# Performance work log

Measured on AMD Instinct MI355X. Metric: run time of the kernel, lower is better.

Reference implementation:

```python
import jax, jax.numpy as jnp
import numpy as np

N_NODES = 50000
N_EDGES = 800000
NFEAT = 128
NHID = 64
NLAYER = 3
BN_EPS = 1e-5


def _bn(h, gamma, beta):
    # BatchNorm1d, training-mode batch statistics (biased variance)
    mu = jnp.mean(h, axis=0)
    var = jnp.mean((h - mu) ** 2, axis=0)
    return gamma * (h - mu) * jax.lax.rsqrt(var + BN_EPS) + beta


def setup_inputs() -> dict:
    key = jax.random.key(0)
    ks = jax.random.split(key, 8)
    x = jax.random.normal(ks[0], (N_NODES, NFEAT), dtype=jnp.float32)
    edge_index = jax.random.randint(ks[1], (2, N_EDGES), 0, N_NODES, dtype=jnp.int64)
    # transform: Linear(nfeat, nhid) with bias, then BN
    W_t = jax.random.normal(ks[2], (NFEAT, NHID), dtype=jnp.float32) / np.sqrt(NFEAT)
    b_t = jnp.zeros((NHID,), dtype=jnp.float32)
    g_t = jnp.ones((NHID,), dtype=jnp.float32)
    bb_t = jnp.zeros((NHID,), dtype=jnp.float32)
    # per-layer GIN MLPs (bias=False) and BN affine params, stacked over layers
    W1 = jax.random.normal(ks[3], (NLAYER, NHID, NHID), dtype=jnp.float32) / np.sqrt(NHID)
    W2 = jax.random.normal(ks[4], (NLAYER, NHID, NHID), dtype=jnp.float32) / np.sqrt(NHID)
    gamma = jnp.ones((NLAYER, NHID), dtype=jnp.float32)
    beta = jnp.zeros((NLAYER, NHID), dtype=jnp.float32)
    return {"x": x, "edge_index": edge_index, "W_t": W_t, "b_t": b_t,
            "g_t": g_t, "bb_t": bb_t, "W1": W1, "W2": W2,
            "gamma": gamma, "beta": beta}


def reference(x, edge_index, W_t, b_t, g_t, bb_t, W1, W2, gamma, beta):
    src, dst = edge_index[0], edge_index[1]
    # input transform: Linear + BN
    h = _bn(x @ W_t + b_t, g_t, bb_t)
    for i in range(NLAYER):
        # dropout p=0 -> identity
        # GINConv (eps=0): (1+eps)*h + sum_{j->i} h_j, then 2-layer MLP
        agg = h + jax.ops.segment_sum(h[src], dst, num_segments=N_NODES)
        h = jax.nn.relu(agg @ W1[i]) @ W2[i]
        h = jax.nn.relu(h)
        h = _bn(h, gamma[i], beta[i])
    # per-graph boolean-mask split is a pure partition of rows; return full matrix
    return h
```

## Files before the change

### kernel.cpp

```cpp
#include <hip/hip_runtime.h>

#define NND 50000
#define NED 800000
#define NF  128
#define NH  64
#define BN_EPS 1e-5
#define NCOPY 64
#define SCB  256
#define NSB  ((NND + SCB - 1) / SCB)

#define WS_HA     0
#define WS_STATS  12800000
#define WS_SSF    (WS_STATS + NCOPY*128*8)
#define WS_DEG    (WS_SSF + 512)
#define WS_OFFS   (WS_DEG + NND*4)
#define WS_CUR    (WS_OFFS + (NND+4)*4)
#define WS_PARTS  (WS_CUR + NND*4)
#define WS_ESRC   (WS_PARTS + 256*4)

__global__ void k_deg(const int* __restrict__ dst, int* __restrict__ deg) {
    int e4 = blockIdx.x * 256 + threadIdx.x;
    if (e4 * 4 < NED) {
        int4 d = ((const int4*)dst)[e4];
        atomicAdd(&deg[d.x], 1);
        atomicAdd(&deg[d.y], 1);
        atomicAdd(&deg[d.z], 1);
        atomicAdd(&deg[d.w], 1);
    }
}

__global__ __launch_bounds__(SCB) void k_part(const int* __restrict__ deg,
                                              int* __restrict__ offs,
                                              int* __restrict__ parts) {
    __shared__ int sd[SCB];
    int t = threadIdx.x;
    int i = blockIdx.x * SCB + t;
    int v = (i < NND) ? deg[i] : 0;
    sd[t] = v;
    __syncthreads();
#pragma unroll
    for (int off = 1; off < SCB; off <<= 1) {
        int u = (t >= off) ? sd[t - off] : 0;
        __syncthreads();
        sd[t] += u;
        __syncthreads();
    }
    if (i < NND) offs[i] = sd[t] - v;
    if (t == SCB - 1) parts[blockIdx.x] = sd[t];
}

__global__ __launch_bounds__(256) void k_scan2(int* __restrict__ parts) {
    __shared__ int sd[256];
    int t = threadIdx.x;
    int v = (t < NSB) ? parts[t] : 0;
    sd[t] = v;
    __syncthreads();
#pragma unroll
    for (int off = 1; off < 256; off <<= 1) {
        int u = (t >= off) ? sd[t - off] : 0;
        __syncthreads();
        sd[t] += u;
        __syncthreads();
    }
    if (t < NSB) parts[t] = sd[t] - v;
}

__global__ __launch_bounds__(256) void k_apply(int* __restrict__ offs,
                                               const int* __restrict__ parts,
                                               int* __restrict__ cur) {
    int i = blockIdx.x * 256 + threadIdx.x;
    if (i < NND) {
        int o = offs[i] + parts[i >> 8];
        offs[i] = o;
        cur[i] = o;
    }
    if (i == NND) offs[NND] = NED;
}

__global__ void k_fill(const int* __restrict__ src, const int* __restrict__ dst,
                       int* __restrict__ cur, int* __restrict__ esrc) {
    int e4 = blockIdx.x * 256 + threadIdx.x;
    if (e4 * 4 < NED) {
        int4 d = ((const int4*)dst)[e4];
        int4 s = ((const int4*)src)[e4];
        esrc[atomicAdd(&cur[d.x], 1)] = s.x;
        esrc[atomicAdd(&cur[d.y], 1)] = s.y;
        esrc[atomicAdd(&cur[d.z], 1)] = s.z;
        esrc[atomicAdd(&cur[d.w], 1)] = s.w;
    }
}

__global__ void k_fin(double* __restrict__ st,
                      const float* __restrict__ g, const float* __restrict__ b,
                      float* __restrict__ ssout) {
    int c = threadIdx.x;
    double sum = 0.0, ssq = 0.0;
    for (int cp = 0; cp < NCOPY; ++cp) {
        sum += st[cp * 128 + c];
        ssq += st[cp * 128 + 64 + c];
    }
    for (int cp = 0; cp < NCOPY; ++cp) {
        st[cp * 128 + c] = 0.0;
        st[cp * 128 + 64 + c] = 0.0;
    }
    double mu  = sum / (double)NND;
    double var = ssq / (double)NND - mu * mu;
    if (var < 0.0) var = 0.0;
    double rs = 1.0 / sqrt(var + BN_EPS);
    double sc = (double)g[c] * rs;
    ssout[c]      = (float)sc;
    ssout[64 + c] = (float)((double)b[c] - mu * sc);
}

__global__ __launch_bounds__(128) void k_transform(const float* __restrict__ x,
                                                   const float* __restrict__ Wt,
                                                   const float* __restrict__ bt,
                                                   float* __restrict__ outraw,
                                                   double* __restrict__ stats) {
    __shared__ __align__(16) float Wl[NF * NH];
    __shared__ __align__(16) float sTbuf[2 * 64 * 68];
    int tid  = threadIdx.x;
    int wave = tid >> 6, lane = tid & 63;
    int ti = lane & 7, tj = lane >> 3;
    int tile = blockIdx.x * 2 + wave;
    int base = tile * 64;
    float* sTw = &sTbuf[wave * 64 * 68];
    const float4* x4 = (const float4*)x;

#pragma unroll
    for (int r = 0; r < 16; ++r) {
        int i4 = r * 128 + tid;
        ((float4*)Wl)[i4] = ((const float4*)Wt)[i4];
    }

    float acc[8][8];
#pragma unroll
    for (int i = 0; i < 8; ++i)
#pragma unroll
        for (int j = 0; j < 8; ++j) acc[i][j] = 0.f;

    for (int ch = 0; ch < 2; ++ch) {
        __syncthreads();
#pragma unroll
        for (int s = 0; s < 16; ++s) {
            int flat = s * 64 + lane;
            int nl = flat >> 4, q = flat & 15;
            float4 v = {0.f, 0.f, 0.f, 0.f};
            if (base + nl < NND) v = x4[(size_t)(base + nl) * 32 + ch * 16 + q];
            sTw[(q * 4 + 0) * 68 + nl] = v.x;
            sTw[(q * 4 + 1) * 68 + nl] = v.y;
            sTw[(q * 4 + 2) * 68 + nl] = v.z;
            sTw[(q * 4 + 3) * 68 + nl] = v.w;
        }
        __syncthreads();
#pragma unroll 2
        for (int k = 0; k < 64; ++k) {
            const float* ap = &sTw[k * 68 + ti * 8];
            float4 alo = *(const float4*)ap;
            float4 ahi = *(const float4*)(ap + 4);
            const float* wp = &Wl[(ch * 64 + k) * NH + tj * 8];
            float4 wlo = *(const float4*)wp;
            float4 whi = *(const float4*)(wp + 4);
            float a8[8] = {alo.x, alo.y, alo.z, alo.w, ahi.x, ahi.y, ahi.z, ahi.w};
            float w8[8] = {wlo.x, wlo.y, wlo.z, wlo.w, whi.x, whi.y, whi.z, whi.w};
#pragma unroll
            for (int i = 0; i < 8; ++i)
#pragma unroll
                for (int j = 0; j < 8; ++j) acc[i][j] += a8[i] * w8[j];
        }
    }

    float b8[8];
    *(float4*)&b8[0] = ((const float4*)bt)[tj * 2];
    *(float4*)&b8[4] = ((const float4*)bt)[tj * 2 + 1];

    float s8[8], q8[8];
#pragma unroll
    for (int j = 0; j < 8; ++j) { s8[j] = 0.f; q8[j] = 0.f; }
#pragma unroll
    for (int i = 0; i < 8; ++i) {
        int n = base + ti * 8 + i;
        if (n < NND) {
            float o[8];
#pragma unroll
            for (int j = 0; j < 8; ++j) {
                o[j] = acc[i][j] + b8[j];
                s8[j] += o[j];
                q8[j] += o[j] * o[j];
            }
            *(float4*)&outraw[(size_t)n * NH + tj * 8]     = *(float4*)&o[0];
            *(float4*)&outraw[(size_t)n * NH + tj * 8 + 4] = *(float4*)&o[4];
        }
    }
#pragma unroll
    for (int m = 1; m < 8; m <<= 1) {
#pragma unroll
        for (int j = 0; j < 8; ++j) {
            s8[j] += __shfl_xor(s8[j], m);
            q8[j] += __shfl_xor(q8[j], m);
        }
    }
    if (ti == 0) {
        int slot = (tile & (NCOPY - 1)) * 128 + tj * 8;
#pragma unroll
        for (int j = 0; j < 8; ++j) {
            atomicAdd(&stats[slot + j], (double)s8[j]);
            atomicAdd(&stats[slot + 64 + j], (double)q8[j]);
        }
    }
}

__global__ __launch_bounds__(256) void k_agg(const float* __restrict__ inraw,
                                             float* __restrict__ aggout,
                                             const float* __restrict__ ss,
                                             const int* __restrict__ offs,
                                             const int* __restrict__ esrc) {
    int tid  = threadIdx.x;
    int lane = tid & 63;
    int wv   = tid >> 6;
    int n = blockIdx.x * 4 + wv;
    int q = lane & 15;
    int r = lane >> 4;
    const float4* in4 = (const float4*)inraw;

    int e0 = offs[n], e1 = offs[n + 1];
    int deg = e1 - e0;

    float4 self = make_float4(0.f, 0.f, 0.f, 0.f);
    if (r == 0) self = in4[(size_t)n * 16 + q];

    float ax = 0.f, ay = 0.f, az = 0.f, aw = 0.f;
    for (int bb = e0; bb < e1; bb += 64) {
        int m = e1 - bb; if (m > 64) m = 64;
        int idx = (lane < m) ? esrc[bb + lane] : 0;
        int t = 0;
        for (; t + 16 <= m; t += 16) {
            int j0 = __shfl(idx, t + r);
            int j1 = __shfl(idx, t + 4 + r);
            int j2 = __shfl(idx, t + 8 + r);
            int j3 = __shfl(idx, t + 12 + r);
            float4 v0 = in4[(size_t)j0 * 16 + q];
            float4 v1 = in4[(size_t)j1 * 16 + q];
            float4 v2 = in4[(size_t)j2 * 16 + q];
            float4 v3 = in4[(size_t)j3 * 16 + q];
            ax += (v0.x + v1.x) + (v2.x + v3.x);
            ay += (v0.y + v1.y) + (v2.y + v3.y);
            az += (v0.z + v1.z) + (v2.z + v3.z);
            aw += (v0.w + v1.w) + (v2.w + v3.w);
        }
        for (; t < m; t += 4) {
            int e = t + r;
            int j = __shfl(idx, e & 63);
            if (e < m) {
                float4 v = in4[(size_t)j * 16 + q];
                ax += v.x; ay += v.y; az += v.z; aw += v.w;
            }
        }
    }

    ax += __shfl_xor(ax, 16); ay += __shfl_xor(ay, 16);
    az += __shfl_xor(az, 16); aw += __shfl_xor(aw, 16);
    ax += __shfl_xor(ax, 32); ay += __shfl_xor(ay, 32);
    az += __shfl_xor(az, 32); aw += __shfl_xor(aw, 32);

    if (r == 0) {
        float4 sc4 = ((const float4*)ss)[q];
        float4 sh4 = ((const float4*)(ss + 64))[q];
        float dn = (float)(deg + 1);
        float4 res;
        res.x = sc4.x * (ax + self.x) + dn * sh4.x;
        res.y = sc4.y * (ay + self.y) + dn * sh4.y;
        res.z = sc4.z * (az + self.z) + dn * sh4.z;
        res.w = sc4.w * (aw + self.w) + dn * sh4.w;
        ((float4*)aggout)[(size_t)n * 16 + q] = res;
    }
}

__global__ __launch_bounds__(128) void k_mlp(float* __restrict__ h,
                                             double* __restrict__ statsout,
                                             const float* __restrict__ W1,
                                             const float* __restrict__ W2) {
    __shared__ __align__(16) float W1l[NH * NH];
    __shared__ __align__(16) float W2l[NH * NH];
    __shared__ __align__(16) float sTbuf[2 * 64 * 68];
    int tid  = threadIdx.x;
    int wave = tid >> 6, lane = tid & 63;
    int ti = lane & 7, tj = lane >> 3;
    int tile = blockIdx.x * 2 + wave;
    int base = tile * 64;
    float* sTw = &sTbuf[wave * 64 * 68];
    const float4* h4 = (const float4*)h;

#pragma unroll
    for (int r = 0; r < 8; ++r) {
        int i4 = r * 128 + tid;
        ((float4*)W1l)[i4] = ((const float4*)W1)[i4];
        ((float4*)W2l)[i4] = ((const float4*)W2)[i4];
    }
#pragma unroll
    for (int s = 0; s < 16; ++s) {
        int flat = s * 64 + lane;
        int nl = flat >> 4, q = flat & 15;
        float4 v = {0.f, 0.f, 0.f, 0.f};
        if (base + nl < NND) v = h4[(size_t)(base + nl) * 16 + q];
        sTw[(q * 4 + 0) * 68 + nl] = v.x;
        sTw[(q * 4 + 1) * 68 + nl] = v.y;
        sTw[(q * 4 + 2) * 68 + nl] = v.z;
        sTw[(q * 4 + 3) * 68 + nl] = v.w;
    }
    __syncthreads();

    float acc[8][8];
#pragma unroll
    for (int i = 0; i < 8; ++i)
#pragma unroll
        for (int j = 0; j < 8; ++j) acc[i][j] = 0.f;
#pragma unroll 2
    for (int k = 0; k < 64; ++k) {
        const float* ap = &sTw[k * 68 + ti * 8];
        float4 alo = *(const float4*)ap;
        float4 ahi = *(const float4*)(ap + 4);
        const float* wp = &W1l[k * NH + tj * 8];
        float4 wlo = *(const float4*)wp;
        float4 whi = *(const float4*)(wp + 4);
        float a8[8] = {alo.x, alo.y, alo.z, alo.w, ahi.x, ahi.y, ahi.z, ahi.w};
        float w8[8] = {wlo.x, wlo.y, wlo.z, wlo.w, whi.x, whi.y, whi.z, whi.w};
#pragma unroll
        for (int i = 0; i < 8; ++i)
#pragma unroll
            for (int j = 0; j < 8; ++j) acc[i][j] += a8[i] * w8[j];
    }
#pragma unroll
    for (int i = 0; i < 8; ++i)
#pragma unroll
        for (int j = 0; j < 8; ++j) acc[i][j] = fmaxf(acc[i][j], 0.f);

    __syncthreads();
#pragma unroll
    for (int j = 0; j < 8; ++j) {
        float* p = &sTw[(tj * 8 + j) * 68 + ti * 8];
        float4 lo = {acc[0][j], acc[1][j], acc[2][j], acc[3][j]};
        float4 hi = {acc[4][j], acc[5][j], acc[6][j], acc[7][j]};
        *(float4*)p = lo;
        *(float4*)(p + 4) = hi;
    }
    __syncthreads();

    float a2[8][8];
#pragma unroll
    for (int i = 0; i < 8; ++i)
#pragma unroll
        for (int j = 0; j < 8; ++j) a2[i][j] = 0.f;
#pragma unroll 2
    for (int k = 0; k < 64; ++k) {
        const float* ap = &sTw[k * 68 + ti * 8];
        float4 alo = *(const float4*)ap;
        float4 ahi = *(const float4*)(ap + 4);
        const float* wp = &W2l[k * NH + tj * 8];
        float4 wlo = *(const float4*)wp;
        float4 whi = *(const float4*)(wp + 4);
        float a8[8] = {alo.x, alo.y, alo.z, alo.w, ahi.x, ahi.y, ahi.z, ahi.w};
        float w8[8] = {wlo.x, wlo.y, wlo.z, wlo.w, whi.x, whi.y, whi.z, whi.w};
#pragma unroll
        for (int i = 0; i < 8; ++i)
#pragma unroll
            for (int j = 0; j < 8; ++j) a2[i][j] += a8[i] * w8[j];
    }

    float s8[8], q8[8];
#pragma unroll
    for (int j = 0; j < 8; ++j) { s8[j] = 0.f; q8[j] = 0.f; }
#pragma unroll
    for (int i = 0; i < 8; ++i) {
        int n = base + ti * 8 + i;
        if (n < NND) {
            float o[8];
#pragma unroll
            for (int j = 0; j < 8; ++j) {
                o[j] = fmaxf(a2[i][j], 0.f);
                s8[j] += o[j];
                q8[j] += o[j] * o[j];
            }
            *(float4*)&h[(size_t)n * NH + tj * 8]     = *(float4*)&o[0];
            *(float4*)&h[(size_t)n * NH + tj * 8 + 4] = *(float4*)&o[4];
        }
    }
#pragma unroll
    for (int m = 1; m < 8; m <<= 1) {
#pragma unroll
        for (int j = 0; j < 8; ++j) {
            s8[j] += __shfl_xor(s8[j], m);
            q8[j] += __shfl_xor(q8[j], m);
        }
    }
    if (ti == 0) {
        int slot = (tile & (NCOPY - 1)) * 128 + tj * 8;
#pragma unroll
        for (int j = 0; j < 8; ++j) {
            atomicAdd(&statsout[slot + j], (double)s8[j]);
            atomicAdd(&statsout[slot + 64 + j], (double)q8[j]);
        }
    }
}

__global__ void k_bnout(float* __restrict__ h, const float* __restrict__ ss) {
    int i4 = blockIdx.x * 256 + threadIdx.x;
    if (i4 < NND * NH / 4) {
        int cg = i4 & 15;
        float4 v   = ((float4*)h)[i4];
        float4 scv = ((const float4*)ss)[cg];
        float4 shv = ((const float4*)(ss + 64))[cg];
        v.x = v.x * scv.x + shv.x;
        v.y = v.y * scv.y + shv.y;
        v.z = v.z * scv.z + shv.z;
        v.w = v.w * scv.w + shv.w;
        ((float4*)h)[i4] = v;
    }
}

extern "C" void kernel_launch(void* const* d_in, const int* in_sizes, int n_in,
                              void* d_out, int out_size, void* d_ws, size_t ws_size,
                              hipStream_t stream) {
    const float* x     = (const float*)d_in[0];
    const int*   ei    = (const int*)d_in[1];
    const float* Wt    = (const float*)d_in[2];
    const float* bt    = (const float*)d_in[3];
    const float* gt    = (const float*)d_in[4];
    const float* bbt   = (const float*)d_in[5];
    const float* W1    = (const float*)d_in[6];
    const float* W2    = (const float*)d_in[7];
    const float* gamma = (const float*)d_in[8];
    const float* beta  = (const float*)d_in[9];
    float* out = (float*)d_out;

    char* ws = (char*)d_ws;
    float*  hA    = (float*)(ws + WS_HA);
    double* stats = (double*)(ws + WS_STATS);
    float*  ssf   = (float*)(ws + WS_SSF);
    int*    deg   = (int*)(ws + WS_DEG);
    int*    offs  = (int*)(ws + WS_OFFS);
    int*    cur   = (int*)(ws + WS_CUR);
    int*    parts = (int*)(ws + WS_PARTS);
    int*    esrc  = (int*)(ws + WS_ESRC);

    const int* srcv = ei;
    const int* dstv = ei + NED;

    hipMemsetAsync(stats, 0, NCOPY * 128 * 8 + 512 + NND * 4, stream);

    const int EB4 = (NED / 4 + 255) / 256;
    k_deg<<<EB4, 256, 0, stream>>>(dstv, deg);
    k_part<<<NSB, SCB, 0, stream>>>(deg, offs, parts);
    k_scan2<<<1, 256, 0, stream>>>(parts);
    k_apply<<<NSB, 256, 0, stream>>>(offs, parts, cur);
    k_fill<<<EB4, 256, 0, stream>>>(srcv, dstv, cur, esrc);

    const int NT2 = 391;
    const int NB  = NND / 4;

    k_transform<<<NT2, 128, 0, stream>>>(x, Wt, bt, hA, stats);
    k_fin<<<1, 64, 0, stream>>>(stats, gt, bbt, ssf);

    k_agg<<<NB, 256, 0, stream>>>(hA, out, ssf, offs, esrc);
    k_mlp<<<NT2, 128, 0, stream>>>(out, stats, W1, W2);
    k_fin<<<1, 64, 0, stream>>>(stats, gamma, beta, ssf);

    k_agg<<<NB, 256, 0, stream>>>(out, hA, ssf, offs, esrc);
    k_mlp<<<NT2, 128, 0, stream>>>(hA, stats, W1 + 4096, W2 + 4096);
    k_fin<<<1, 64, 0, stream>>>(stats, gamma + 64, beta + 64, ssf);

    k_agg<<<NB, 256, 0, stream>>>(hA, out, ssf, offs, esrc);
    k_mlp<<<NT2, 128, 0, stream>>>(out, stats, W1 + 8192, W2 + 8192);
    k_fin<<<1, 64, 0, stream>>>(stats, gamma + 128, beta + 128, ssf);

    k_bnout<<<(NND * NH / 4 + 255) / 256, 256, 0, stream>>>(out, ssf);
}
```

Before: 330.3 us.

## Partition degree and CSR-fill atomics by XCD-owned destination node ranges

```diff
diff --git a/kernel.cpp b/kernel.cpp
--- a/kernel.cpp
+++ b/kernel.cpp
@@ -8,6 +8,8 @@
 #define NCOPY 64
 #define SCB  256
 #define NSB  ((NND + SCB - 1) / SCB)
+#define XNODES (NND / 8)
+#define FCH  196
 
 #define WS_HA     0
 #define WS_STATS  12800000
@@ -18,14 +20,44 @@
 #define WS_PARTS  (WS_CUR + NND*4)
 #define WS_ESRC   (WS_PARTS + 256*4)
 
-__global__ void k_deg(const int* __restrict__ dst, int* __restrict__ deg) {
-    int e4 = blockIdx.x * 256 + threadIdx.x;
-    if (e4 * 4 < NED) {
-        int4 d = ((const int4*)dst)[e4];
-        atomicAdd(&deg[d.x], 1);
-        atomicAdd(&deg[d.y], 1);
-        atomicAdd(&deg[d.z], 1);
-        atomicAdd(&deg[d.w], 1);
+__global__ __launch_bounds__(256) void k_deg(const int* __restrict__ dst,
+                                             int* __restrict__ deg) {
+    int xcd = blockIdx.x & 7;
+    int chunk = blockIdx.x >> 3;
+    int lo = xcd * XNODES;
+    const int4* d4 = (const int4*)dst;
+#pragma unroll
+    for (int r = 0; r < 4; ++r) {
+        int i = chunk * 1024 + r * 256 + threadIdx.x;
+        if (i < NED / 4) {
+            int4 d = d4[i];
+            if ((unsigned)(d.x - lo) < XNODES) atomicAdd(&deg[d.x], 1);
+            if ((unsigned)(d.y - lo) < XNODES) atomicAdd(&deg[d.y], 1);
+            if ((unsigned)(d.z - lo) < XNODES) atomicAdd(&deg[d.z], 1);
+            if ((unsigned)(d.w - lo) < XNODES) atomicAdd(&deg[d.w], 1);
+        }
+    }
+}
+
+__global__ __launch_bounds__(256) void k_fill(const int* __restrict__ src,
+                                              const int* __restrict__ dst,
+                                              int* __restrict__ cur,
+                                              int* __restrict__ esrc) {
+    int xcd = blockIdx.x & 7;
+    int chunk = blockIdx.x >> 3;
+    int lo = xcd * XNODES;
+    const int4* d4 = (const int4*)dst;
+#pragma unroll
+    for (int r = 0; r < 4; ++r) {
+        int i = chunk * 1024 + r * 256 + threadIdx.x;
+        if (i < NED / 4) {
+            int4 d = d4[i];
+            int e = i * 4;
+            if ((unsigned)(d.x - lo) < XNODES) esrc[atomicAdd(&cur[d.x], 1)] = src[e];
+            if ((unsigned)(d.y - lo) < XNODES) esrc[atomicAdd(&cur[d.y], 1)] = src[e + 1];
+            if ((unsigned)(d.z - lo) < XNODES) esrc[atomicAdd(&cur[d.z], 1)] = src[e + 2];
+            if ((unsigned)(d.w - lo) < XNODES) esrc[atomicAdd(&cur[d.w], 1)] = src[e + 3];
+        }
     }
 }
 
@@ -75,19 +107,6 @@
         cur[i] = o;
     }
     if (i == NND) offs[NND] = NED;
-}
-
-__global__ void k_fill(const int* __restrict__ src, const int* __restrict__ dst,
-                       int* __restrict__ cur, int* __restrict__ esrc) {
-    int e4 = blockIdx.x * 256 + threadIdx.x;
-    if (e4 * 4 < NED) {
-        int4 d = ((const int4*)dst)[e4];
-        int4 s = ((const int4*)src)[e4];
-        esrc[atomicAdd(&cur[d.x], 1)] = s.x;
-        esrc[atomicAdd(&cur[d.y], 1)] = s.y;
-        esrc[atomicAdd(&cur[d.z], 1)] = s.z;
-        esrc[atomicAdd(&cur[d.w], 1)] = s.w;
-    }
 }
 
 __global__ void k_fin(double* __restrict__ st,
@@ -448,12 +467,12 @@
 
     hipMemsetAsync(stats, 0, NCOPY * 128 * 8 + 512 + NND * 4, stream);
 
-    const int EB4 = (NED / 4 + 255) / 256;
-    k_deg<<<EB4, 256, 0, stream>>>(dstv, deg);
+    const int PGRID = FCH * 8;
+    k_deg<<<PGRID, 256, 0, stream>>>(dstv, deg);
     k_part<<<NSB, SCB, 0, stream>>>(deg, offs, parts);
     k_scan2<<<1, 256, 0, stream>>>(parts);
     k_apply<<<NSB, 256, 0, stream>>>(offs, parts, cur);
-    k_fill<<<EB4, 256, 0, stream>>>(srcv, dstv, cur, esrc);
+    k_fill<<<PGRID, 256, 0, stream>>>(srcv, dstv, cur, esrc);
 
     const int NT2 = 391;
     const int NB  = NND / 4;
```

Result: faster. 321.4 us (-2.7%).
